# Kernel tuning notes

Measured on AMD Instinct MI355X. Metric: run time of the kernel, lower is better.

Reference implementation:

```python
import jax, jax.numpy as jnp
import numpy as np
from jax import lax

# ---- static config (matches init_kwargs) ----
B, D, H, HD, MLP = 64, 768, 12, 64, 3072
DEPTH = 11                     # trunk blocks; block 12 is used (twice) as b1/b2
IMG_H, IMG_W, P, S = 256, 128, 16, 12
NY, NX = (IMG_H - P) // S + 1, (IMG_W - P) // S + 1   # 21, 10
NP = NY * NX                   # 210 patches
N = NP + 1                     # +CLS = 211 tokens
NUM_CIDS = 8
SCALE = HD ** -0.5
SIE = 3.0                      # sie_xishu
SHIFT, GROUPS, DIV = 5, 2, 4
EPS = 1e-6
_PNAMES = ["ln1_g", "ln1_b", "qkv_w", "qkv_b", "proj_w", "proj_b",
           "ln2_g", "ln2_b", "fc1_w", "fc1_b", "fc2_w", "fc2_b"]


def layernorm(x, g, b):
    m = jnp.mean(x, -1, keepdims=True)
    v = jnp.mean(jnp.square(x - m), -1, keepdims=True)
    return (x - m) * lax.rsqrt(v + EPS) * g + b


def block(x, p):
    """Pre-norm ViT block: manual attention (q@k.T softmax @v) + GELU MLP."""
    ln1g, ln1b, qkvw, qkvb, projw, projb, ln2g, ln2b, fc1w, fc1b, fc2w, fc2b = p
    Bn, Nn = x.shape[0], x.shape[1]
    h = layernorm(x, ln1g, ln1b)
    qkv = (h @ qkvw + qkvb).reshape(Bn, Nn, 3, H, HD)
    q, k, v = qkv[:, :, 0], qkv[:, :, 1], qkv[:, :, 2]           # [B,N,H,HD]
    attn = jax.nn.softmax(jnp.einsum('bnhd,bmhd->bhnm', q * SCALE, k), axis=-1)
    o = jnp.einsum('bhnm,bmhd->bnhd', attn, v).reshape(Bn, Nn, D)
    x = x + o @ projw + projb
    h = layernorm(x, ln2g, ln2b)
    return x + jax.nn.gelu(h @ fc1w + fc1b, approximate=False) @ fc2w + fc2b


def _block_params(k, lead=()):
    ks = jax.random.split(k, 4)
    z = lambda s: jnp.zeros(lead + s, jnp.float32)
    o = lambda s: jnp.ones(lead + s, jnp.float32)
    r = lambda kk, s, fan: jax.random.normal(kk, lead + s, jnp.float32) * (fan ** -0.5)
    return dict(ln1_g=o((D,)), ln1_b=z((D,)),
                qkv_w=r(ks[0], (D, 3 * D), D), qkv_b=z((3 * D,)),
                proj_w=r(ks[1], (D, D), D), proj_b=z((D,)),
                ln2_g=o((D,)), ln2_b=z((D,)),
                fc1_w=r(ks[2], (D, MLP), D), fc1_b=z((MLP,)),
                fc2_w=r(ks[3], (MLP, D), MLP), fc2_b=z((D,)))


def setup_inputs() -> dict:
    key = jax.random.key(0)
    k = jax.random.split(key, 8)
    inp = {
        "x": jax.random.normal(k[0], (B, 3, IMG_H, IMG_W), jnp.float32),
        "cids": jax.random.randint(k[1], (B,), 0, NUM_CIDS),
        "conv_w": jax.random.normal(k[2], (D, 3, P, P), jnp.float32) * np.float32(np.sqrt(2.0 / (P * P * D))),
        "conv_b": jnp.zeros((D,), jnp.float32),
        "cls_token": jax.random.normal(k[3], (1, 1, D), jnp.float32) * 0.02,
        "pos_embed": jax.random.normal(k[4], (1, N, D), jnp.float32) * 0.02,
        "sie_embed": jax.random.normal(k[5], (NUM_CIDS, 1, D), jnp.float32) * 0.02,
    }
    for name, arr in _block_params(k[6], (DEPTH,)).items():
        inp["blk_" + name] = arr
    for pre, kk in (("b1_", jax.random.fold_in(key, 101)), ("b2_", jax.random.fold_in(key, 102))):
        for name, arr in _block_params(kk).items():
            inp[pre + name] = arr
        inp[pre + "norm_g"] = jnp.ones((D,), jnp.float32)
        inp[pre + "norm_b"] = jnp.zeros((D,), jnp.float32)
    return inp


def reference(x, cids, conv_w, conv_b, cls_token, pos_embed, sie_embed,
              blk_ln1_g, blk_ln1_b, blk_qkv_w, blk_qkv_b, blk_proj_w, blk_proj_b,
              blk_ln2_g, blk_ln2_b, blk_fc1_w, blk_fc1_b, blk_fc2_w, blk_fc2_b,
              b1_ln1_g, b1_ln1_b, b1_qkv_w, b1_qkv_b, b1_proj_w, b1_proj_b,
              b1_ln2_g, b1_ln2_b, b1_fc1_w, b1_fc1_b, b1_fc2_w, b1_fc2_b,
              b1_norm_g, b1_norm_b,
              b2_ln1_g, b2_ln1_b, b2_qkv_w, b2_qkv_b, b2_proj_w, b2_proj_b,
              b2_ln2_g, b2_ln2_b, b2_fc1_w, b2_fc1_b, b2_fc2_w, b2_fc2_b,
              b2_norm_g, b2_norm_b):
    Bn = x.shape[0]
    # overlapping patch embed: Conv2d(3->768, k=16, s=12), flatten, transpose
    y = lax.conv_general_dilated(x, conv_w, (S, S), 'VALID',
                                 dimension_numbers=('NCHW', 'OIHW', 'NCHW'))
    y = (y + conv_b[None, :, None, None]).reshape(Bn, D, NP).transpose(0, 2, 1)
    t = jnp.concatenate([jnp.broadcast_to(cls_token, (Bn, 1, D)), y], axis=1)
    t = t + pos_embed + SIE * sie_embed[cids]   # SIE camera embedding
    # 11 trunk blocks via scan over stacked params
    stk = (blk_ln1_g, blk_ln1_b, blk_qkv_w, blk_qkv_b, blk_proj_w, blk_proj_b,
           blk_ln2_g, blk_ln2_b, blk_fc1_w, blk_fc1_b, blk_fc2_w, blk_fc2_b)
    t = lax.scan(lambda c, p: (block(c, p), None), t, stk)[0]
    # global branch: b1 = block12 + final norm, take CLS
    b1p = (b1_ln1_g, b1_ln1_b, b1_qkv_w, b1_qkv_b, b1_proj_w, b1_proj_b,
           b1_ln2_g, b1_ln2_b, b1_fc1_w, b1_fc1_b, b1_fc2_w, b1_fc2_b)
    f0 = layernorm(block(t, b1p), b1_norm_g, b1_norm_b)[:, 0]
    # shuffle_unit(t, shift=5, group=2, begin=1) -> jigsaw rearranged patches [B,210,D]
    xs = jnp.concatenate([t[:, SHIFT:], t[:, 1:SHIFT]], axis=1)
    xs = xs.reshape(Bn, GROUPS, -1, D).transpose(0, 2, 1, 3).reshape(Bn, -1, D)
    token = t[:, 0:1]
    pl = NP // DIV                                   # 52
    b2p = (b2_ln1_g, b2_ln1_b, b2_qkv_w, b2_qkv_b, b2_proj_w, b2_proj_b,
           b2_ln2_g, b2_ln2_b, b2_fc1_w, b2_fc1_b, b2_fc2_w, b2_fc2_b)
    feats = [f0]
    for i in range(DIV):
        seg = jnp.concatenate([token, xs[:, i * pl:(i + 1) * pl]], axis=1)   # [B,53,D]
        feats.append(layernorm(block(seg, b2p), b2_norm_g, b2_norm_b)[:, 0])
    # eval output with neck_feat='before': necks pass features through;
    # concat global + local/divide_length -> [B, 5*768]
    return jnp.concatenate([feats[0]] + [f / DIV for f in feats[1:]], axis=1)
```

## Files before the change

### kernel.cpp

```cpp
#include <hip/hip_runtime.h>
#include <hip/hip_bf16.h>
#include <cstdint>
#include <cstddef>
#include <math.h>

using bf16 = __hip_bfloat16;
typedef __bf16 bf16x8 __attribute__((ext_vector_type(8)));
typedef float f32x4 __attribute__((ext_vector_type(4)));

static constexpr int NHEAD = 12;
static constexpr int NTOK  = 211;
static constexpr int DEPTH = 11;

static __device__ __forceinline__ void gload_lds16(const bf16* g, bf16* lds) {
  __builtin_amdgcn_global_load_lds(
      (const __attribute__((address_space(1))) uint32_t*)g,
      (__attribute__((address_space(3))) uint32_t*)lds,
      16, 0, 0);
}

__device__ __forceinline__ float gelu_f(float x) {
  float u = x * (0.7978845608f + 0.0356774081f * x * x);
  float t = 1.f - 2.f / (__expf(2.f * u) + 1.f);
  return 0.5f * x * (1.f + t);
}

static __device__ __forceinline__ unsigned short bf16_bits(float x) {
  return __builtin_bit_cast(unsigned short, __float2bfloat16(x));
}

static __device__ __forceinline__ int b2src(int row) {
  int bb = row / 53, jj = row - bb * 53;
  int i = bb >> 6, b = bb & 63;
  int src;
  if (jj == 0) src = 0;
  else {
    int jx = i * 52 + (jj - 1);
    int mm = (jx & 1) * 105 + (jx >> 1);
    src = (mm < 206) ? (5 + mm) : (1 + (mm - 206));
  }
  return b * 211 + src;
}

template <bool GELU, bool RES, typename CT, int OUT>
__global__ __launch_bounds__(256) void gemm_db(
    const bf16* __restrict__ A, const bf16* __restrict__ Bt,
    const float* __restrict__ bias, const float* __restrict__ res,
    CT* __restrict__ C, int M, int N, int K, int gn, int sA, int sR, int sC,
    bf16* __restrict__ qh, bf16* __restrict__ kh, bf16* __restrict__ vh,
    int pad, int ntd, int coff)
{
  __shared__ bf16 sb[2][8192];

  const int tid = threadIdx.x;
  const int w = tid >> 6, l = tid & 63;
  const int lr = l & 15, lg = l >> 4;
  const int wr = (w >> 1) * 64, wc = (w & 1) * 64;

  const int nwg = gridDim.x, lin = blockIdx.x;
  const int q = nwg >> 3, r = nwg & 7;
  const int xcd = lin & 7, pos = lin >> 3;
  const int wg = (xcd < r ? xcd * (q + 1) : r * (q + 1) + (xcd - r) * q) + pos;
  const int bm0 = (wg / gn) * 128, bn0 = (wg % gn) * 128;

  f32x4 acc[4][4];
#pragma unroll
  for (int i = 0; i < 4; ++i)
#pragma unroll
    for (int j = 0; j < 4; ++j) acc[i][j] = f32x4{0.f, 0.f, 0.f, 0.f};

  size_t aof[2], bof[2]; int dst[2];
#pragma unroll
  for (int j = 0; j < 2; ++j) {
    const int c = j * 256 + tid;
    const int row = c >> 2;
    const int ch = (c & 3) ^ ((row >> 1) & 3);
    int ar = bm0 + row; if (ar >= M) ar = M - 1;
    aof[j] = (size_t)ar * sA + ch * 8;
    bof[j] = (size_t)(bn0 + row) * K + ch * 8;
    dst[j] = c * 8;
  }

  const int nt = K >> 5;

  auto stage = [&](int t) {
    bf16* s = sb[t & 1];
    const size_t ko = (size_t)t * 32;
    gload_lds16(A + aof[0] + ko, s + dst[0]);
    gload_lds16(A + aof[1] + ko, s + dst[1]);
    gload_lds16(Bt + bof[0] + ko, s + 4096 + dst[0]);
    gload_lds16(Bt + bof[1] + ko, s + 4096 + dst[1]);
  };

  stage(0);
  __syncthreads();

  const int swz = (lg ^ ((lr >> 1) & 3)) * 8;

  for (int t = 0; t < nt; ++t) {
    if (t + 1 < nt) stage(t + 1);
    const bf16* As = sb[t & 1];
    const bf16* Bs = As + 4096;
    bf16x8 af[4], bv[4];
#pragma unroll
    for (int mi = 0; mi < 4; ++mi)
      af[mi] = *(const bf16x8*)(As + (wr + mi * 16 + lr) * 32 + swz);
#pragma unroll
    for (int ni = 0; ni < 4; ++ni)
      bv[ni] = *(const bf16x8*)(Bs + (wc + ni * 16 + lr) * 32 + swz);
#pragma unroll
    for (int mi = 0; mi < 4; ++mi)
#pragma unroll
      for (int ni = 0; ni < 4; ++ni)
        acc[mi][ni] = __builtin_amdgcn_mfma_f32_16x16x32_bf16(af[mi], bv[ni], acc[mi][ni], 0, 0, 0);
    __syncthreads();
  }

  if constexpr (OUT == 2 || sizeof(CT) == 2) {
    char* lb = (char*)sb;
#pragma unroll
    for (int mi = 0; mi < 4; ++mi) {
#pragma unroll
      for (int ni = 0; ni < 4; ++ni) {
        const int cloc = wc + ni * 16 + lr;
        const float bvl = bias[bn0 + cloc];
#pragma unroll
        for (int r2 = 0; r2 < 4; ++r2) {
          const int rowl = wr + mi * 16 + lg * 4 + r2;
          float v = acc[mi][ni][r2] + bvl;
          if constexpr (GELU) v = gelu_f(v);
          *(unsigned short*)(lb + rowl * 256 + ((cloc * 2) ^ (((rowl >> 1) & 6) << 4))) =
              bf16_bits(v);
        }
      }
    }
    __syncthreads();
#pragma unroll
    for (int j = 0; j < 8; ++j) {
      const int flat = j * 256 + tid;
      const int row = flat >> 4, ch = flat & 15;
      const int grow = bm0 + row;
      if (grow < M) {
        const f32x4 v = *(const f32x4*)(lb + row * 256 + ((ch * 16) ^ (((row >> 1) & 6) << 4)));
        if constexpr (OUT == 2) {
          const int col0 = bn0 + ch * 8 + coff;
          const int region = (col0 >= 1536) ? 2 : (col0 >= 768 ? 1 : 0);
          const int c7 = col0 - region * 768;
          const int h = c7 >> 6, d = c7 & 63;
          const int bb2 = grow / ntd;
          const int tok = grow - bb2 * ntd;
          bf16* db = (region == 0) ? qh : ((region == 1) ? kh : vh);
          *(f32x4*)((char*)db + (((size_t)(bb2 * 12 + h) * pad + tok) * 64 + d) * 2) = v;
        } else {
          *(f32x4*)((char*)C + ((size_t)grow * sC + bn0 + ch * 8) * 2) = v;
        }
      }
    }
  } else {
#pragma unroll
    for (int mi = 0; mi < 4; ++mi) {
#pragma unroll
      for (int ni = 0; ni < 4; ++ni) {
        const int col = bn0 + wc + ni * 16 + lr;
        const float bvl = bias[col];
#pragma unroll
        for (int r2 = 0; r2 < 4; ++r2) {
          const int row = bm0 + wr + mi * 16 + lg * 4 + r2;
          if (row < M) {
            float v = acc[mi][ni][r2] + bvl;
            if constexpr (GELU) v = gelu_f(v);
            if constexpr (RES) v += res[(size_t)row * sR + col];
            C[(size_t)row * sC + col] = v;
          }
        }
      }
    }
  }
}

__global__ __launch_bounds__(256) void vtrans_kernel(
    const bf16* __restrict__ vcomp, bf16* __restrict__ vT, int ntok, int pad)
{
  __shared__ unsigned short t[224 * 65];
  const int bb = blockIdx.x, h = blockIdx.y;
  const unsigned short* src = (const unsigned short*)vcomp + (size_t)(bb * 12 + h) * pad * 64;
  for (int idx = threadIdx.x; idx < ntok * 64; idx += 256) {
    int tok = idx >> 6, d = idx & 63;
    t[tok * 65 + d] = src[idx];
  }
  __syncthreads();
  unsigned short* dstp = (unsigned short*)vT + (size_t)(bb * 12 + h) * 64 * pad;
  for (int idx = threadIdx.x; idx < 64 * ntok; idx += 256) {
    int d = idx / ntok, tok = idx - d * ntok;
    dstp[(size_t)d * pad + tok] = t[tok * 65 + d];
  }
}

template <int NKF, bool ONLY0>
__global__ __launch_bounds__(256) void attn_kernel(
    const bf16* __restrict__ qb, const bf16* __restrict__ kb,
    const bf16* __restrict__ vsrc, bf16* __restrict__ ao, int ntok, int pad)
{
  constexpr int NPAD = NKF * 16;
  constexpr int VST = NPAD + 8;
  __shared__ bf16 Pl[4][16][NPAD];
  __shared__ __bf16 Vt[ONLY0 ? 1 : 64][ONLY0 ? 1 : VST];
  const int bb = blockIdx.x;
  const int h = blockIdx.y;
  const int tid = threadIdx.x;
  const int w = tid >> 6, l = tid & 63;
  const int lr = l & 15, lg = l >> 4;
  const int bbh = bb * 12 + h;
  const __bf16* qbase = reinterpret_cast<const __bf16*>(qb) + (size_t)bbh * pad * 64;
  const __bf16* kbase = reinterpret_cast<const __bf16*>(kb) + (size_t)bbh * pad * 64;
  const __bf16* vglob = reinterpret_cast<const __bf16*>(vsrc) +
                        (ONLY0 ? (size_t)bbh * 64 * pad : (size_t)bbh * pad * 64);

  if constexpr (!ONLY0) {
    for (int idx = tid; idx < ntok * 64; idx += 256) {
      const int tok = idx >> 6, d = idx & 63;
      Vt[d][tok] = vglob[idx];
    }
    __syncthreads();
  }
  if (ONLY0 && w > 0) return;

  for (int qt = w; qt < (ONLY0 ? 1 : NKF); qt += 4) {
    int qrow = qt * 16 + lr; if (qrow >= ntok) qrow = ntok - 1;
    const __bf16* qp = qbase + qrow * 64 + lg * 8;
    const bf16x8 qf0 = *reinterpret_cast<const bf16x8*>(qp);
    const bf16x8 qf1 = *reinterpret_cast<const bf16x8*>(qp + 32);

    f32x4 s[NKF];
#pragma unroll
    for (int kf = 0; kf < NKF; ++kf) {
      int krow = kf * 16 + lr; if (krow >= ntok) krow = ntok - 1;
      const __bf16* kp = kbase + krow * 64 + lg * 8;
      f32x4 a = f32x4{0.f, 0.f, 0.f, 0.f};
      a = __builtin_amdgcn_mfma_f32_16x16x32_bf16(qf0, *reinterpret_cast<const bf16x8*>(kp), a, 0, 0, 0);
      a = __builtin_amdgcn_mfma_f32_16x16x32_bf16(qf1, *reinterpret_cast<const bf16x8*>(kp + 32), a, 0, 0, 0);
      s[kf] = a;
    }

    float rs[4];
#pragma unroll
    for (int r = 0; r < 4; ++r) {
      float mx = -1e30f;
#pragma unroll
      for (int kf = 0; kf < NKF; ++kf)
        if (kf * 16 + lr < ntok) mx = fmaxf(mx, s[kf][r]);
#pragma unroll
      for (int d = 1; d < 16; d <<= 1) mx = fmaxf(mx, __shfl_xor(mx, d));
      float sum = 0.f;
#pragma unroll
      for (int kf = 0; kf < NKF; ++kf) {
        float p = 0.f;
        if (kf * 16 + lr < ntok) p = __expf((s[kf][r] - mx) * 0.125f);
        sum += p;
        Pl[w][lg * 4 + r][kf * 16 + lr] = __float2bfloat16(p);
      }
#pragma unroll
      for (int d = 1; d < 16; d <<= 1) sum += __shfl_xor(sum, d);
      rs[r] = sum;
    }
    __builtin_amdgcn_s_waitcnt(0);

    f32x4 o[4];
#pragma unroll
    for (int ni = 0; ni < 4; ++ni) o[ni] = f32x4{0.f, 0.f, 0.f, 0.f};
#pragma unroll
    for (int ks = 0; ks < NPAD / 32; ++ks) {
      const bf16x8 pa = *reinterpret_cast<const bf16x8*>(&Pl[w][lr][ks * 32 + lg * 8]);
#pragma unroll
      for (int ni = 0; ni < 4; ++ni) {
        bf16x8 vb;
        if constexpr (ONLY0) {
          vb = *reinterpret_cast<const bf16x8*>(
              vglob + (size_t)(ni * 16 + lr) * pad + ks * 32 + lg * 8);
        } else {
          vb = *reinterpret_cast<const bf16x8*>(&Vt[ni * 16 + lr][ks * 32 + lg * 8]);
        }
        o[ni] = __builtin_amdgcn_mfma_f32_16x16x32_bf16(pa, vb, o[ni], 0, 0, 0);
      }
    }
#pragma unroll
    for (int ni = 0; ni < 4; ++ni)
#pragma unroll
      for (int r = 0; r < 4; ++r) {
        int qq = qt * 16 + lg * 4 + r;
        if (qq < (ONLY0 ? 1 : ntok)) {
          float val = o[ni][r] / rs[r];
          ao[((size_t)bb * ntok + qq) * 768 + h * 64 + ni * 16 + lr] = __float2bfloat16(val);
        }
      }
  }
}

static __device__ __forceinline__ void ln_row2(
    const float* __restrict__ xrow, const float* __restrict__ g, const float* __restrict__ b,
    bf16* __restrict__ outrow, int l)
{
  const float4* xr = reinterpret_cast<const float4*>(xrow);
  float4 v[3]; float s = 0.f;
#pragma unroll
  for (int i = 0; i < 3; ++i) {
    v[i] = xr[l + i * 64];
    s += v[i].x + v[i].y + v[i].z + v[i].w;
  }
#pragma unroll
  for (int d = 1; d < 64; d <<= 1) s += __shfl_xor(s, d);
  float mean = s * (1.f / 768.f);
  float s2 = 0.f;
#pragma unroll
  for (int i = 0; i < 3; ++i) {
    float a0 = v[i].x - mean, a1 = v[i].y - mean, a2 = v[i].z - mean, a3 = v[i].w - mean;
    s2 += a0 * a0 + a1 * a1 + a2 * a2 + a3 * a3;
  }
#pragma unroll
  for (int d = 1; d < 64; d <<= 1) s2 += __shfl_xor(s2, d);
  float rstd = rsqrtf(s2 * (1.f / 768.f) + 1e-6f);
  const float4* g4 = reinterpret_cast<const float4*>(g);
  const float4* b4 = reinterpret_cast<const float4*>(b);
  unsigned short* orow = reinterpret_cast<unsigned short*>(outrow);
#pragma unroll
  for (int i = 0; i < 3; ++i) {
    float4 gg = g4[l + i * 64], bb = b4[l + i * 64];
    ushort4 pk;
    pk.x = bf16_bits((v[i].x - mean) * rstd * gg.x + bb.x);
    pk.y = bf16_bits((v[i].y - mean) * rstd * gg.y + bb.y);
    pk.z = bf16_bits((v[i].z - mean) * rstd * gg.z + bb.z);
    pk.w = bf16_bits((v[i].w - mean) * rstd * gg.w + bb.w);
    *reinterpret_cast<ushort4*>(orow + (l + i * 64) * 4) = pk;
  }
}

__global__ __launch_bounds__(256) void ln_kernel(
    const float* __restrict__ x, const float* __restrict__ g, const float* __restrict__ b,
    bf16* __restrict__ out, int Mrows)
{
  int row = blockIdx.x * 4 + (threadIdx.x >> 6);
  if (row >= Mrows) return;
  ln_row2(x + (size_t)row * 768, g, b, out + (size_t)row * 768, threadIdx.x & 63);
}

__global__ __launch_bounds__(256) void tln_kernel(
    const float* __restrict__ w0, const float* __restrict__ w1,
    const float* __restrict__ w2, const float* __restrict__ w3,
    bf16* __restrict__ d0, bf16* __restrict__ d1,
    bf16* __restrict__ d2, bf16* __restrict__ d3,
    const float* __restrict__ x, const float* __restrict__ g,
    const float* __restrict__ b, bf16* __restrict__ outh, int Mrows,
    int gmode, float* __restrict__ rdst, int nr)
{
  __shared__ float tile[32][33];
  int id = blockIdx.x;
  if (id >= 6912) {
    const int lnb = (Mrows + 3) / 4;
    int seg = id - 6912;
    if (seg < lnb) {
      int row = seg * 4 + (threadIdx.x >> 6);
      if (row < Mrows) {
        int srow = gmode ? b2src(row) : row;
        ln_row2(x + (size_t)srow * 768, g, b, outh + (size_t)row * 768, threadIdx.x & 63);
      }
    } else {
      int rr = (seg - lnb) * 4 + (threadIdx.x >> 6);
      if (rr < nr) {
        const int l = threadIdx.x & 63;
        const float4* src4 = reinterpret_cast<const float4*>(x + (size_t)(rr & 63) * 211 * 768);
        float4* dst4 = reinterpret_cast<float4*>(rdst + (size_t)rr * 768);
#pragma unroll
        for (int i = 0; i < 3; ++i) dst4[l + i * 64] = src4[l + i * 64];
      }
    }
    return;
  }
  const float* in; bf16* out; int R, C, tt;
  if (id < 1728)      { in = w0; out = d0; R = 768;  C = 2304; tt = id; }
  else if (id < 2304) { in = w1; out = d1; R = 768;  C = 768;  tt = id - 1728; }
  else if (id < 4608) { in = w2; out = d2; R = 768;  C = 3072; tt = id - 2304; }
  else                { in = w3; out = d3; R = 3072; C = 768;  tt = id - 4608; }
  const int tc = C >> 5;
  int c0 = (tt % tc) * 32, r0 = (tt / tc) * 32;
  int tx = threadIdx.x & 31, ty = threadIdx.x >> 5;
#pragma unroll
  for (int i = 0; i < 4; ++i) {
    int rr = ty + i * 8;
    tile[rr][tx] = in[(size_t)(r0 + rr) * C + c0 + tx];
  }
  __syncthreads();
#pragma unroll
  for (int i = 0; i < 4; ++i) {
    int c = ty + i * 8;
    out[(size_t)(c0 + c) * R + r0 + tx] = __float2bfloat16(tile[tx][c]);
  }
}

__global__ __launch_bounds__(256) void ln_head_kernel(
    const float* __restrict__ x, int tokstride, const float* __restrict__ g,
    const float* __restrict__ b, float* __restrict__ out, int nbb, int mode)
{
  int bb = blockIdx.x * 4 + (threadIdx.x >> 6);
  if (bb >= nbb) return;
  int l = threadIdx.x & 63;
  const float* xr = x + (size_t)bb * tokstride * 768;
  float v[12]; float s = 0.f;
#pragma unroll
  for (int i = 0; i < 12; ++i) { v[i] = xr[l + i * 64]; s += v[i]; }
#pragma unroll
  for (int d = 1; d < 64; d <<= 1) s += __shfl_xor(s, d);
  float mean = s * (1.f / 768.f);
  float s2 = 0.f;
#pragma unroll
  for (int i = 0; i < 12; ++i) { float t = v[i] - mean; s2 += t * t; }
#pragma unroll
  for (int d = 1; d < 64; d <<= 1) s2 += __shfl_xor(s2, d);
  float rstd = rsqrtf(s2 * (1.f / 768.f) + 1e-6f);
  float scale = mode ? 0.25f : 1.f;
  int b_ = mode ? (bb & 63) : bb;
  int off = mode ? (1 + (bb >> 6)) * 768 : 0;
  float* orow = out + (size_t)b_ * 3840 + off;
#pragma unroll
  for (int i = 0; i < 12; ++i) {
    orow[l + i * 64] = ((v[i] - mean) * rstd * g[l + i * 64] + b[l + i * 64]) * scale;
  }
}

__global__ void prep_kernel(const float* __restrict__ x, bf16* __restrict__ pm,
                            const float* __restrict__ convw, bf16* __restrict__ cw)
{
  int idx = blockIdx.x * 256 + threadIdx.x;
  if (idx < 13440 * 768) {
    int k = idx % 768;
    int m = idx / 768;
    int b = m / 210, p = m % 210;
    int py = p / 10, px = p % 10;
    int c = k >> 8, ij = k & 255, i = ij >> 4, j = ij & 15;
    pm[idx] = __float2bfloat16(x[(((size_t)b * 3 + c) * 256 + py * 12 + i) * 128 + px * 12 + j]);
  } else {
    int idx2 = idx - 13440 * 768;
    if (idx2 < 768 * 768) cw[idx2] = __float2bfloat16(convw[idx2]);
  }
}

__global__ void assemble_kernel(
    const bf16* __restrict__ y, const float* __restrict__ cls, const float* __restrict__ pos,
    const float* __restrict__ sie, const int* __restrict__ cids, float* __restrict__ tA)
{
  int idx = blockIdx.x * 256 + threadIdx.x;
  if (idx >= 13504 * 768) return;
  int d = idx % 768;
  int t = (idx / 768) % 211;
  int b = idx / (768 * 211);
  float v = pos[t * 768 + d] + 3.0f * sie[cids[b] * 768 + d];
  if (t == 0) v += cls[d];
  else v += __bfloat162float(y[((size_t)b * 210 + (t - 1)) * 768 + d]);
  tA[idx] = v;
}

struct BlkP {
  const float *ln1_g, *ln1_b, *qkv_w, *qkv_b, *proj_w, *proj_b;
  const float *ln2_g, *ln2_b, *fc1_w, *fc1_b, *fc2_w, *fc2_b;
};

extern "C" void kernel_launch(void* const* d_in, const int* in_sizes, int n_in,
                              void* d_out, int out_size, void* d_ws, size_t ws_size,
                              hipStream_t stream)
{
  (void)in_sizes; (void)n_in; (void)out_size; (void)ws_size;
  const float* xin   = (const float*)d_in[0];
  const int*   cids  = (const int*)  d_in[1];
  const float* convw = (const float*)d_in[2];
  const float* convb = (const float*)d_in[3];
  const float* cls   = (const float*)d_in[4];
  const float* pos   = (const float*)d_in[5];
  const float* sie   = (const float*)d_in[6];
  float* out = (float*)d_out;

  char* ws = (char*)d_ws;
  bf16*  qkvT = (bf16*)(ws + 0);
  bf16*  projT = (bf16*)(ws + 3538944);
  bf16*  fc1T = (bf16*)(ws + 4718592);
  bf16*  fc2T = (bf16*)(ws + 9437184);
  float* tA   = (float*)(ws + 14155776);
  float* rcb  = (float*)(ws + 55640064);
  bf16*  hb   = (bf16*)(ws + 97320960);
  bf16*  qb   = (bf16*)(ws + 118161408);
  bf16*  kb   = (bf16*)(ws + 143327232);
  bf16*  vb   = (bf16*)(ws + 168493056);
  bf16*  big  = (bf16*)(ws + 118161408);
  char*  sbuf = ws + 193658880;
  float* y0   = (float*)(sbuf);
  bf16*  hb0  = (bf16*)(sbuf + 786432);
  bf16*  big0 = (bf16*)(sbuf + 1179648);
  float* f0b  = (float*)(sbuf + 2752512);
  bf16*  ao   = (bf16*)(ws + 201523200);
  bf16*  vTb  = (bf16*)(ws + 222363648);

  dim3 blk(256);

  auto apply_block = [&](float* xbuf, const BlkP& p, int nb, int ntok_) {
    const int M = nb * ntok_;
    const int gm = (M + 127) / 128;
    const int pad = (ntok_ == NTOK) ? 224 : 64;
    tln_kernel<<<dim3(6912 + (M + 3) / 4), blk, 0, stream>>>(
        p.qkv_w, p.proj_w, p.fc1_w, p.fc2_w, qkvT, projT, fc1T, fc2T,
        xbuf, p.ln1_g, p.ln1_b, hb, M, 0, nullptr, 0);
    gemm_db<false, false, bf16, 2><<<dim3(gm * 18), blk, 0, stream>>>(
        hb, qkvT, p.qkv_b, nullptr, (bf16*)nullptr, M, 2304, 768, 18, 768, 0, 0,
        qb, kb, vb, pad, ntok_, 0);
    attn_kernel<14, false><<<dim3(nb, NHEAD), blk, 0, stream>>>(qb, kb, vb, ao, ntok_, pad);
    gemm_db<false, true, float, 0><<<dim3(gm * 6), blk, 0, stream>>>(
        ao, projT, p.proj_b, xbuf, xbuf, M, 768, 768, 6, 768, 768, 768,
        nullptr, nullptr, nullptr, 0, 1, 0);
    ln_kernel<<<dim3((M + 3) / 4), blk, 0, stream>>>(xbuf, p.ln2_g, p.ln2_b, hb, M);
    gemm_db<true, false, bf16, 0><<<dim3(gm * 24), blk, 0, stream>>>(
        hb, fc1T, p.fc1_b, nullptr, big, M, 3072, 768, 24, 768, 3072, 3072,
        nullptr, nullptr, nullptr, 0, 1, 0);
    gemm_db<false, true, float, 0><<<dim3(gm * 6), blk, 0, stream>>>(
        big, fc2T, p.fc2_b, xbuf, xbuf, M, 768, 3072, 6, 3072, 768, 768,
        nullptr, nullptr, nullptr, 0, 1, 0);
  };

  auto apply_head_block = [&](const float* xsrc, const BlkP& p, int nb, int ntok_,
                              const float* ng, const float* nbias, int mode,
                              int gmode, const float* resp, int rstride) {
    const int M = nb * ntok_;
    const int gm = (M + 127) / 128;
    const int gm0 = (nb + 127) / 128;
    const int pad = (ntok_ == NTOK) ? 224 : 64;
    const int nr = gmode ? nb : 0;
    tln_kernel<<<dim3(6912 + (M + 3) / 4 + (nr + 3) / 4), blk, 0, stream>>>(
        p.qkv_w, p.proj_w, p.fc1_w, p.fc2_w, qkvT, projT, fc1T, fc2T,
        xsrc, p.ln1_g, p.ln1_b, hb, M, gmode, rcb, nr);
    gemm_db<false, false, bf16, 2><<<dim3(gm * 12), blk, 0, stream>>>(
        hb, qkvT + 768 * 768, p.qkv_b + 768, nullptr, (bf16*)nullptr,
        M, 1536, 768, 12, 768, 0, 0, qb, kb, vb, pad, ntok_, 768);
    gemm_db<false, false, bf16, 2><<<dim3(gm0 * 6), blk, 0, stream>>>(
        hb, qkvT, p.qkv_b, nullptr, (bf16*)nullptr,
        nb, 768, 768, 6, ntok_ * 768, 0, 0, qb, kb, vb, pad, 1, 0);
    vtrans_kernel<<<dim3(nb, NHEAD), blk, 0, stream>>>(vb, vTb, ntok_, pad);
    if (ntok_ == NTOK)
      attn_kernel<14, true><<<dim3(nb, NHEAD), blk, 0, stream>>>(qb, kb, vTb, ao, ntok_, pad);
    else
      attn_kernel<4, true><<<dim3(nb, NHEAD), blk, 0, stream>>>(qb, kb, vTb, ao, ntok_, pad);
    gemm_db<false, true, float, 0><<<dim3(gm0 * 6), blk, 0, stream>>>(
        ao, projT, p.proj_b, resp, y0, nb, 768, 768, 6, ntok_ * 768, rstride, 768,
        nullptr, nullptr, nullptr, 0, 1, 0);
    ln_kernel<<<dim3((nb + 3) / 4), blk, 0, stream>>>(y0, p.ln2_g, p.ln2_b, hb0, nb);
    gemm_db<true, false, bf16, 0><<<dim3(gm0 * 24), blk, 0, stream>>>(
        hb0, fc1T, p.fc1_b, nullptr, big0, nb, 3072, 768, 24, 768, 3072, 3072,
        nullptr, nullptr, nullptr, 0, 1, 0);
    gemm_db<false, true, float, 0><<<dim3(gm0 * 6), blk, 0, stream>>>(
        big0, fc2T, p.fc2_b, y0, f0b, nb, 768, 3072, 6, 3072, 768, 768,
        nullptr, nullptr, nullptr, 0, 1, 0);
    ln_head_kernel<<<dim3((nb + 3) / 4), blk, 0, stream>>>(
        f0b, 1, ng, nbias, out, nb, mode);
  };

  {
    int total = 13440 * 768 + 768 * 768;
    prep_kernel<<<dim3((total + 255) / 256), blk, 0, stream>>>(xin, big, convw, qkvT);
    gemm_db<false, false, bf16, 0><<<dim3(105 * 6), blk, 0, stream>>>(
        big, qkvT, convb, nullptr, ao, 13440, 768, 768, 6, 768, 768, 768,
        nullptr, nullptr, nullptr, 0, 1, 0);
    total = 13504 * 768;
    assemble_kernel<<<dim3((total + 255) / 256), blk, 0, stream>>>(ao, cls, pos, sie, cids, tA);
  }

  const float* bp[12];
  for (int i = 0; i < 12; ++i) bp[i] = (const float*)d_in[7 + i];
  for (int dd = 0; dd < DEPTH; ++dd) {
    BlkP p;
    p.ln1_g = bp[0] + dd * 768;                p.ln1_b = bp[1] + dd * 768;
    p.qkv_w = bp[2] + (size_t)dd * 768 * 2304; p.qkv_b = bp[3] + dd * 2304;
    p.proj_w = bp[4] + (size_t)dd * 768 * 768; p.proj_b = bp[5] + dd * 768;
    p.ln2_g = bp[6] + dd * 768;                p.ln2_b = bp[7] + dd * 768;
    p.fc1_w = bp[8] + (size_t)dd * 768 * 3072; p.fc1_b = bp[9] + dd * 3072;
    p.fc2_w = bp[10] + (size_t)dd * 3072 * 768; p.fc2_b = bp[11] + dd * 768;
    apply_block(tA, p, 64, NTOK);
  }

  {
    BlkP p;
    p.ln1_g = (const float*)d_in[19]; p.ln1_b = (const float*)d_in[20];
    p.qkv_w = (const float*)d_in[21]; p.qkv_b = (const float*)d_in[22];
    p.proj_w = (const float*)d_in[23]; p.proj_b = (const float*)d_in[24];
    p.ln2_g = (const float*)d_in[25]; p.ln2_b = (const float*)d_in[26];
    p.fc1_w = (const float*)d_in[27]; p.fc1_b = (const float*)d_in[28];
    p.fc2_w = (const float*)d_in[29]; p.fc2_b = (const float*)d_in[30];
    apply_head_block(tA, p, 64, NTOK,
                     (const float*)d_in[31], (const float*)d_in[32], 0,
                     0, tA, NTOK * 768);
  }

  {
    BlkP p;
    p.ln1_g = (const float*)d_in[33]; p.ln1_b = (const float*)d_in[34];
    p.qkv_w = (const float*)d_in[35]; p.qkv_b = (const float*)d_in[36];
    p.proj_w = (const float*)d_in[37]; p.proj_b = (const float*)d_in[38];
    p.ln2_g = (const float*)d_in[39]; p.ln2_b = (const float*)d_in[40];
    p.fc1_w = (const float*)d_in[41]; p.fc1_b = (const float*)d_in[42];
    p.fc2_w = (const float*)d_in[43]; p.fc2_b = (const float*)d_in[44];
    apply_head_block(tA, p, 256, 53,
                     (const float*)d_in[45], (const float*)d_in[46], 1,
                     1, rcb, 768);
  }
}
```

Before: 4.870 ms.

## Transpose MFMA operands for vectorized epilogue stores and drop XCD remap

Swaps the A and B operands of the MFMA so each lane holds four consecutive columns of one row. The epilogue can then use 16-byte bias loads, packed 8-byte LDS writes and f32x4 residual loads and output stores in place of scalar ones. The LDS swizzle is changed to match. The XCD-aware workgroup remapping is also removed in favour of plain blockIdx order, which may lower L2 locality across chiplets.

```diff
diff --git a/kernel.cpp b/kernel.cpp
--- a/kernel.cpp
+++ b/kernel.cpp
@@ -57,10 +57,7 @@
   const int lr = l & 15, lg = l >> 4;
   const int wr = (w >> 1) * 64, wc = (w & 1) * 64;
 
-  const int nwg = gridDim.x, lin = blockIdx.x;
-  const int q = nwg >> 3, r = nwg & 7;
-  const int xcd = lin & 7, pos = lin >> 3;
-  const int wg = (xcd < r ? xcd * (q + 1) : r * (q + 1) + (xcd - r) * q) + pos;
+  const int wg = blockIdx.x;
   const int bm0 = (wg / gn) * 128, bn0 = (wg % gn) * 128;
 
   f32x4 acc[4][4];
@@ -112,7 +109,7 @@
     for (int mi = 0; mi < 4; ++mi)
 #pragma unroll
       for (int ni = 0; ni < 4; ++ni)
-        acc[mi][ni] = __builtin_amdgcn_mfma_f32_16x16x32_bf16(af[mi], bv[ni], acc[mi][ni], 0, 0, 0);
+        acc[mi][ni] = __builtin_amdgcn_mfma_f32_16x16x32_bf16(bv[ni], af[mi], acc[mi][ni], 0, 0, 0);
     __syncthreads();
   }
 
@@ -120,18 +117,20 @@
     char* lb = (char*)sb;
 #pragma unroll
     for (int mi = 0; mi < 4; ++mi) {
+      const int rowl = wr + mi * 16 + lr;
+      const int rx = (rowl & 7) << 4;
 #pragma unroll
       for (int ni = 0; ni < 4; ++ni) {
-        const int cloc = wc + ni * 16 + lr;
-        const float bvl = bias[bn0 + cloc];
+        const int colb = wc + ni * 16 + lg * 4;
+        const f32x4 b4 = *(const f32x4*)(bias + bn0 + colb);
+        ushort4 pk;
 #pragma unroll
         for (int r2 = 0; r2 < 4; ++r2) {
-          const int rowl = wr + mi * 16 + lg * 4 + r2;
-          float v = acc[mi][ni][r2] + bvl;
+          float v = acc[mi][ni][r2] + b4[r2];
           if constexpr (GELU) v = gelu_f(v);
-          *(unsigned short*)(lb + rowl * 256 + ((cloc * 2) ^ (((rowl >> 1) & 6) << 4))) =
-              bf16_bits(v);
+          ((unsigned short*)&pk)[r2] = bf16_bits(v);
         }
+        *(ushort4*)(lb + rowl * 256 + ((colb * 2) ^ rx)) = pk;
       }
     }
     __syncthreads();
@@ -141,7 +140,7 @@
       const int row = flat >> 4, ch = flat & 15;
       const int grow = bm0 + row;
       if (grow < M) {
-        const f32x4 v = *(const f32x4*)(lb + row * 256 + ((ch * 16) ^ (((row >> 1) & 6) << 4)));
+        const f32x4 v = *(const f32x4*)(lb + row * 256 + ((ch * 16) ^ ((row & 7) << 4)));
         if constexpr (OUT == 2) {
           const int col0 = bn0 + ch * 8 + coff;
           const int region = (col0 >= 1536) ? 2 : (col0 >= 768 ? 1 : 0);
@@ -159,19 +158,18 @@
   } else {
 #pragma unroll
     for (int mi = 0; mi < 4; ++mi) {
-#pragma unroll
-      for (int ni = 0; ni < 4; ++ni) {
-        const int col = bn0 + wc + ni * 16 + lr;
-        const float bvl = bias[col];
-#pragma unroll
-        for (int r2 = 0; r2 < 4; ++r2) {
-          const int row = bm0 + wr + mi * 16 + lg * 4 + r2;
-          if (row < M) {
-            float v = acc[mi][ni][r2] + bvl;
-            if constexpr (GELU) v = gelu_f(v);
-            if constexpr (RES) v += res[(size_t)row * sR + col];
-            C[(size_t)row * sC + col] = v;
+      const int row = bm0 + wr + mi * 16 + lr;
+      if (row < M) {
+#pragma unroll
+        for (int ni = 0; ni < 4; ++ni) {
+          const int col0 = bn0 + wc + ni * 16 + lg * 4;
+          f32x4 v = acc[mi][ni] + *(const f32x4*)(bias + col0);
+          if constexpr (GELU) {
+#pragma unroll
+            for (int r2 = 0; r2 < 4; ++r2) v[r2] = gelu_f(v[r2]);
           }
+          if constexpr (RES) v += *(const f32x4*)(res + (size_t)row * sR + col0);
+          *(f32x4*)((float*)C + (size_t)row * sC + col0) = v;
         }
       }
     }
```

Result: no change. 4.959 ms (+1.8%).
